# Optimization experiments

Measured on AMD Instinct MI355X. Metric: run time of the kernel, lower is better.

The kernel has to match this reference:

```python
import jax, jax.numpy as jnp
import numpy as np

B, L, D, NHEADS, P = 64, 256, 768, 8, 3
VOCAB, DEP, NLAYERS = 30522, 45, 2
LAM = 0.5


def _forward(src_mask, aspect_mask, lex, attention_mask,
             tok_emb, seg_emb, pool_w, pool_b, ln_a, ln_b,
             dep_emb, fc1_w, fc1_b, fc2_w, fc2_b,
             aq_w, aq_b, ak_w, ak_b, lq_w, lq_b, lk_w, lk_b, root_w,
             gcn_w, gcn_b, fc3_w, fc3_b, cls_w, cls_b, vlin_w,
             text_bert_indices, bert_segments_ids, ori_tag, head):
    b, l = text_bert_indices.shape
    d = tok_emb.shape[1]
    dk = d // NHEADS
    NEG = jnp.float32(-1e30)
    # stand-in BERT encoder: token + segment embeddings, tanh pooler on [CLS]
    seq = tok_emb[text_bert_indices] + seg_emb[bert_segments_ids]
    pooled = jnp.tanh(seq[:, 0] @ pool_w + pool_b)
    # torch LayerNorm variant: unbiased std (ddof=1)
    mean = seq.mean(-1, keepdims=True)
    std = jnp.std(seq, axis=-1, keepdims=True, ddof=1)
    gcn_in = ln_a * (seq - mean) / (std + 1e-6) + ln_b
    # in-place fmask[:,0]=1 mutates src_mask storage in torch -> effective mask
    sm = src_mask.at[:, 0].set(1.0)
    # dependency-tag score -> per-token softmax -> scatter into [L,L] adjacency
    dep_h = jax.nn.relu(dep_emb[ori_tag] @ fc1_w + fc1_b)
    dep_s = (dep_h @ fc2_w + fc2_b)[..., 0]                      # [B,L]
    dep_feat = jax.nn.softmax(dep_s * sm + (1.0 - sm) * NEG, axis=1)
    to_idx = jnp.arange(1, l)
    fro = head[:, :l - 1]                                        # [B,L-1]
    b_idx = jnp.arange(b)[:, None]
    vals = dep_feat[:, :l - 1]
    dep_adj = jnp.ones((b, l, l), jnp.float32)
    dep_adj = dep_adj.at[b_idx, fro, to_idx[None, :]].set(vals)
    dep_adj = dep_adj.at[b_idx, to_idx[None, :], fro].set(vals)
    # multi-head attention-as-adjacency (returns softmax weights only)
    q = (gcn_in @ aq_w + aq_b).reshape(b, l, NHEADS, dk).transpose(0, 2, 1, 3)
    k = (gcn_in @ ak_w + ak_b).reshape(b, l, NHEADS, dk).transpose(0, 2, 1, 3)
    scores = jnp.einsum('bhqd,bhkd->bhqk', q, k) / (jnp.sqrt(jnp.float32(dk)) + 1e-9)
    scores = jnp.where(sm[:, None, None, :] == 0, jnp.float32(-1e9), scores)
    adj_ag = jax.nn.softmax(scores, axis=-1).mean(axis=1)        # [B,L,L]
    eye = jnp.eye(l, dtype=jnp.float32)
    adj_ag = (adj_ag * (1.0 - eye) + eye) * sm[:, :, None]
    # structured latent attention (stand-in for missing StructuredAtt):
    # masked bilinear attention biased by dep_adj + root attention loss
    q2 = gcn_in @ lq_w + lq_b
    k2 = gcn_in @ lk_w + lk_b
    lat = jnp.einsum('bqd,bkd->bqk', q2, k2) / jnp.sqrt(jnp.float32(d))
    lat = lat + dep_adj + (1.0 - sm)[:, None, :] * (-10000.0)
    adj_latent = jax.nn.softmax(lat, axis=-1)
    root_p = jax.nn.softmax((gcn_in @ root_w)[..., 0] * sm + (1.0 - sm) * NEG, axis=1)
    loss_root = -jnp.mean(jnp.log(jnp.sum(root_p * aspect_mask, axis=1) + 1e-9))
    adj_latent = (adj_latent * (1.0 - eye) + eye) * sm[:, :, None]
    # gated dual-adjacency GCN layers
    H_l = gcn_in
    I_sem = gcn_in
    for layer in range(gcn_w.shape[0]):
        g_l = jax.nn.sigmoid(H_l)
        I_sem = (adj_ag @ H_l) @ gcn_w[layer] + gcn_b[layer]
        I_lat = (adj_latent @ H_l) @ gcn_w[layer] + gcn_b[layer]
        g = jax.nn.sigmoid(I_lat)
        lam_g = LAM * g
        I_com = (1.0 - lam_g) * I_sem + lam_g * I_lat
        H_out = jax.nn.relu(I_com @ fc3_w + fc3_b)
        H_l = g_l * H_out + (1.0 - g_l) * H_l
    # readout
    asp_wn = aspect_mask.sum(axis=1, keepdims=True)              # [B,1]
    m3 = sm[:, :, None]
    h_l = H_l * m3
    h_sem = I_sem * m3
    beta = jnp.einsum('bqd,bkd->bqk', h_l, h_sem) / 1000.0
    attn_o = jax.nn.softmax(beta.sum(axis=1, keepdims=True), axis=2)  # [B,1,L]
    outputs = (attn_o @ I_sem)[:, 0]                             # [B,D]
    sem_pool = (I_sem * aspect_mask[:, :, None]).sum(axis=1) / (asp_wn + 1e-9)
    final = jnp.concatenate([outputs, sem_pool, pooled], axis=-1)  # [B,3D]
    logits = final @ cls_w + cls_b
    e = (H_l @ vlin_w)[..., 0]
    lw = jax.nn.softmax(e, axis=1) * 50.0
    lw = lw * sm.at[:, 0].set(0.0)
    lexicon_loss = jnp.mean((lw - lex) ** 2)
    return logits, loss_root, lexicon_loss


def setup_inputs() -> dict:
    key = jax.random.key(0)
    ks = jax.random.split(key, 24)
    s = 0.02
    n = lambda i, shape: jax.random.normal(ks[i], shape, dtype=jnp.float32) * s
    inp = {}
    inp['text_bert_indices'] = jax.random.randint(ks[0], (B, L), 0, VOCAB, dtype=jnp.int32)
    inp['bert_segments_ids'] = jnp.zeros((B, L), jnp.int32)
    inp['attention_mask'] = jnp.ones((B, L), jnp.float32)
    inp['src_mask'] = jnp.ones((B, L), jnp.float32)
    inp['aspect_mask'] = jax.random.randint(ks[1], (B, L), 0, 2).astype(jnp.float32)
    inp['lex'] = jax.random.uniform(ks[2], (B, L), dtype=jnp.float32)
    inp['ori_tag'] = jax.random.randint(ks[3], (B, L), 0, DEP, dtype=jnp.int32)
    inp['head'] = jax.random.randint(ks[4], (B, L), 0, L, dtype=jnp.int32)
    inp['tok_emb'] = n(5, (VOCAB, D)); inp['seg_emb'] = n(6, (2, D))
    inp['pool_w'] = n(7, (D, D)); inp['pool_b'] = jnp.zeros((D,), jnp.float32)
    inp['ln_a'] = jnp.ones((D,), jnp.float32); inp['ln_b'] = jnp.zeros((D,), jnp.float32)
    inp['dep_emb'] = n(8, (DEP, 300))
    inp['fc1_w'] = n(9, (300, 256)); inp['fc1_b'] = jnp.zeros((256,), jnp.float32)
    inp['fc2_w'] = n(10, (256, 1)); inp['fc2_b'] = jnp.zeros((1,), jnp.float32)
    inp['aq_w'] = n(11, (D, D)); inp['aq_b'] = jnp.zeros((D,), jnp.float32)
    inp['ak_w'] = n(12, (D, D)); inp['ak_b'] = jnp.zeros((D,), jnp.float32)
    inp['lq_w'] = n(13, (D, D)); inp['lq_b'] = jnp.zeros((D,), jnp.float32)
    inp['lk_w'] = n(14, (D, D)); inp['lk_b'] = jnp.zeros((D,), jnp.float32)
    inp['root_w'] = n(15, (D, 1))
    inp['gcn_w'] = n(16, (NLAYERS, D, D)); inp['gcn_b'] = jnp.zeros((NLAYERS, D), jnp.float32)
    inp['fc3_w'] = n(17, (D, D)); inp['fc3_b'] = jnp.zeros((D,), jnp.float32)
    inp['cls_w'] = n(18, (3 * D, P)); inp['cls_b'] = jnp.zeros((P,), jnp.float32)
    inp['vlin_w'] = n(19, (D, 1))
    return inp


def reference(text_bert_indices, bert_segments_ids, attention_mask, src_mask, aspect_mask, lex,
              ori_tag, head, tok_emb, seg_emb, pool_w, pool_b, ln_a, ln_b, dep_emb,
              fc1_w, fc1_b, fc2_w, fc2_b, aq_w, aq_b, ak_w, ak_b, lq_w, lq_b, lk_w, lk_b,
              root_w, gcn_w, gcn_b, fc3_w, fc3_b, cls_w, cls_b, vlin_w):
    return _forward(src_mask, aspect_mask, lex, attention_mask,
                    tok_emb, seg_emb, pool_w, pool_b, ln_a, ln_b,
                    dep_emb, fc1_w, fc1_b, fc2_w, fc2_b,
                    aq_w, aq_b, ak_w, ak_b, lq_w, lq_b, lk_w, lk_b, root_w,
                    gcn_w, gcn_b, fc3_w, fc3_b, cls_w, cls_b, vlin_w,
                    text_bert_indices, bert_segments_ids, ori_tag, head)
```

## Files before the change

kernel.cpp:

```cpp
#include <hip/hip_runtime.h>
#include <hip/hip_bf16.h>
#include <math.h>

#define DI __device__ __forceinline__

constexpr int cB = 64, cL = 256, cD = 768;
constexpr long BLD = (long)cB * cL * cD;
constexpr long BLL = (long)cB * cL * cL;
constexpr long cLL = (long)cL * cL;
constexpr long cLD = (long)cL * cD;

typedef __attribute__((ext_vector_type(8))) short b8;
typedef __attribute__((ext_vector_type(4))) float f4;

#define GLDS(g, l)                                                    \
  __builtin_amdgcn_global_load_lds(                                   \
      (const __attribute__((address_space(1))) void*)(g),             \
      (__attribute__((address_space(3))) void*)(l), 16, 0, 0)

DI float wsum(float v) {
#pragma unroll
  for (int o = 32; o > 0; o >>= 1) v += __shfl_down(v, o, 64);
  return v;
}
DI float wsum_all(float v) {
#pragma unroll
  for (int m = 32; m > 0; m >>= 1) v += __shfl_xor(v, m, 64);
  return v;
}
DI float wmax_all(float v) {
#pragma unroll
  for (int m = 32; m > 0; m >>= 1) v = fmaxf(v, __shfl_xor(v, m, 64));
  return v;
}
DI float wmaxr(float v) {
#pragma unroll
  for (int o = 32; o > 0; o >>= 1) v = fmaxf(v, __shfl_down(v, o, 64));
  return v;
}
DI float blockSum(float v) {
  __shared__ float sh[4];
  v = wsum(v);
  __syncthreads();
  if ((threadIdx.x & 63) == 0) sh[threadIdx.x >> 6] = v;
  __syncthreads();
  return sh[0] + sh[1] + sh[2] + sh[3];
}
DI float blockMax(float v) {
  __shared__ float sh[4];
  v = wmaxr(v);
  __syncthreads();
  if ((threadIdx.x & 63) == 0) sh[threadIdx.x >> 6] = v;
  __syncthreads();
  return fmaxf(fmaxf(sh[0], sh[1]), fmaxf(sh[2], sh[3]));
}
DI float sigf(float x) { return 1.f / (1.f + expf(-x)); }

template <int OBF, int RELU, int BIAS, int EPI>
__global__ __launch_bounds__(256, 2) void bgemm(
    const __hip_bfloat16* __restrict__ A, const __hip_bfloat16* __restrict__ BT,
    void* __restrict__ Cv, const float* __restrict__ bias,
    float* __restrict__ auxf, __hip_bfloat16* __restrict__ auxb,
    int K, int lda, int ldb, int ldc,
    int zshift, int zmask, long sA1, long sA2, long sB1, long sB2, long sC,
    int czdiv) {
  __shared__ __hip_bfloat16 Asp[128 * 32];
  __shared__ __hip_bfloat16 Bsp[128 * 32];
  int z = blockIdx.z;
  A += (long)(z >> zshift) * sA1 + (long)(z & zmask) * sA2;
  BT += (long)(z >> zshift) * sB1 + (long)(z & zmask) * sB2;
  int tid = threadIdx.x;
  int lane = tid & 63, w = tid >> 6;
  int wr = w >> 1, wc = w & 1;
  int l16 = lane & 15, q = lane >> 4;
  int m0 = blockIdx.y << 7, n0 = blockIdx.x << 7;

  int fm = tid >> 2, fq = tid & 3;
  const __hip_bfloat16* Ap0 = A + (long)(m0 + fm) * lda + fq * 8;
  const __hip_bfloat16* Ap1 = A + (long)(m0 + fm + 64) * lda + fq * 8;
  const __hip_bfloat16* Bp0 = BT + (long)(n0 + fm) * ldb + fq * 8;
  const __hip_bfloat16* Bp1 = BT + (long)(n0 + fm + 64) * ldb + fq * 8;
  char* Aw0 = (char*)Asp + (w << 10);
  char* Aw1 = (char*)Asp + 4096 + (w << 10);
  char* Bw0 = (char*)Bsp + (w << 10);
  char* Bw1 = (char*)Bsp + 4096 + (w << 10);

  f4 acc[4][4];
#pragma unroll
  for (int i = 0; i < 4; i++)
#pragma unroll
    for (int j = 0; j < 4; j++) acc[i][j] = (f4){0.f, 0.f, 0.f, 0.f};

  for (int k0 = 0; k0 < K; k0 += 32) {
    GLDS(Ap0 + k0, Aw0);
    GLDS(Ap1 + k0, Aw1);
    GLDS(Bp0 + k0, Bw0);
    GLDS(Bp1 + k0, Bw1);
    __syncthreads();
    b8 af[4], bf[4];
#pragma unroll
    for (int i = 0; i < 4; i++)
      af[i] = *(const b8*)&Asp[(wr * 64 + i * 16 + l16) * 32 + q * 8];
#pragma unroll
    for (int j = 0; j < 4; j++)
      bf[j] = *(const b8*)&Bsp[(wc * 64 + j * 16 + l16) * 32 + q * 8];
#pragma unroll
    for (int i = 0; i < 4; i++)
#pragma unroll
      for (int j = 0; j < 4; j++)
        acc[i][j] = __builtin_amdgcn_mfma_f32_16x16x32_bf16(af[i], bf[j], acc[i][j], 0, 0, 0);
    __syncthreads();
  }
  if (EPI == 4) {
#pragma unroll
    for (int j = 0; j < 4; j++) {
      int n = n0 + wc * 64 + j * 16 + l16;
#pragma unroll
      for (int i = 0; i < 4; i++) {
        int m = m0 + wr * 64 + i * 16 + (q << 2);
        __hip_bfloat16 t4[4];
#pragma unroll
        for (int r = 0; r < 4; r++) t4[r] = __float2bfloat16(acc[i][j][r]);
        long bidx = (long)(m >> 8) * sC + (long)n * cL + (m & 255);
        *(uint2*)&((__hip_bfloat16*)Cv)[bidx] = *(uint2*)t4;
      }
    }
    return;
  }
  long cz = (long)(z >> czdiv) * sC;
#pragma unroll
  for (int j = 0; j < 4; j++) {
    int n = n0 + wc * 64 + j * 16 + l16;
    float bv = BIAS ? bias[n] : 0.f;
#pragma unroll
    for (int i = 0; i < 4; i++) {
#pragma unroll
      for (int r = 0; r < 4; r++) {
        int m = m0 + wr * 64 + i * 16 + q * 4 + r;
        long idx = cz + (long)m * ldc + n;
        float v = acc[i][j][r] + bv;
        if (EPI == 0) {
          if (RELU) v = fmaxf(v, 0.f);
          if (OBF)
            ((__hip_bfloat16*)Cv)[idx] = __float2bfloat16(v);
          else
            ((float*)Cv)[idx] = v;
        } else {
          v = fmaxf(v, 0.f);
          float h = __bfloat162float(auxb[idx]);
          float g = sigf(h);
          float o = h + g * (v - h);
          auxb[idx] = __float2bfloat16(o);
          if (auxf) auxf[idx] = o;
        }
      }
    }
  }
}

__global__ __launch_bounds__(256, 2) void bgemm_dual(
    const __hip_bfloat16* __restrict__ A1g, const __hip_bfloat16* __restrict__ A2g,
    const __hip_bfloat16* __restrict__ BTg, float* __restrict__ IsemF,
    __hip_bfloat16* __restrict__ Icb, const float* __restrict__ bias,
    int write_isem) {
  __shared__ __hip_bfloat16 A1sp[128 * 32];
  __shared__ __hip_bfloat16 A2sp[128 * 32];
  __shared__ __hip_bfloat16 Bsp[128 * 32];
  int z = blockIdx.z;
  const __hip_bfloat16* A1 = A1g + (long)z * cLL;
  const __hip_bfloat16* A2 = A2g + (long)z * cLL;
  const __hip_bfloat16* BT = BTg + (long)z * cLD;
  int tid = threadIdx.x;
  int lane = tid & 63, w = tid >> 6;
  int wr = w >> 1, wc = w & 1;
  int l16 = lane & 15, q = lane >> 4;
  int m0 = blockIdx.y << 7, n0 = blockIdx.x << 7;

  int fm = tid >> 2, fq = tid & 3;
  const __hip_bfloat16* A1p0 = A1 + (long)(m0 + fm) * cL + fq * 8;
  const __hip_bfloat16* A1p1 = A1p0 + 64L * cL;
  const __hip_bfloat16* A2p0 = A2 + (long)(m0 + fm) * cL + fq * 8;
  const __hip_bfloat16* A2p1 = A2p0 + 64L * cL;
  const __hip_bfloat16* Bp0 = BT + (long)(n0 + fm) * cL + fq * 8;
  const __hip_bfloat16* Bp1 = Bp0 + 64L * cL;
  char* w10 = (char*)A1sp + (w << 10);
  char* w11 = (char*)A1sp + 4096 + (w << 10);
  char* w20 = (char*)A2sp + (w << 10);
  char* w21 = (char*)A2sp + 4096 + (w << 10);
  char* wb0 = (char*)Bsp + (w << 10);
  char* wb1 = (char*)Bsp + 4096 + (w << 10);

  f4 ac1[4][4], ac2[4][4];
#pragma unroll
  for (int i = 0; i < 4; i++)
#pragma unroll
    for (int j = 0; j < 4; j++) {
      ac1[i][j] = (f4){0.f, 0.f, 0.f, 0.f};
      ac2[i][j] = (f4){0.f, 0.f, 0.f, 0.f};
    }

  for (int k0 = 0; k0 < cL; k0 += 32) {
    GLDS(A1p0 + k0, w10);
    GLDS(A1p1 + k0, w11);
    GLDS(A2p0 + k0, w20);
    GLDS(A2p1 + k0, w21);
    GLDS(Bp0 + k0, wb0);
    GLDS(Bp1 + k0, wb1);
    __syncthreads();
    b8 a1f[4], a2f[4], bf[4];
#pragma unroll
    for (int i = 0; i < 4; i++) {
      a1f[i] = *(const b8*)&A1sp[(wr * 64 + i * 16 + l16) * 32 + q * 8];
      a2f[i] = *(const b8*)&A2sp[(wr * 64 + i * 16 + l16) * 32 + q * 8];
    }
#pragma unroll
    for (int j = 0; j < 4; j++)
      bf[j] = *(const b8*)&Bsp[(wc * 64 + j * 16 + l16) * 32 + q * 8];
#pragma unroll
    for (int i = 0; i < 4; i++)
#pragma unroll
      for (int j = 0; j < 4; j++) {
        ac1[i][j] = __builtin_amdgcn_mfma_f32_16x16x32_bf16(a1f[i], bf[j], ac1[i][j], 0, 0, 0);
        ac2[i][j] = __builtin_amdgcn_mfma_f32_16x16x32_bf16(a2f[i], bf[j], ac2[i][j], 0, 0, 0);
      }
    __syncthreads();
  }
  long cz = (long)z * cLD;
#pragma unroll
  for (int j = 0; j < 4; j++) {
    int n = n0 + wc * 64 + j * 16 + l16;
    float bv = bias[n];
#pragma unroll
    for (int i = 0; i < 4; i++) {
#pragma unroll
      for (int r = 0; r < 4; r++) {
        int m = m0 + wr * 64 + i * 16 + q * 4 + r;
        long idx = cz + (long)m * cD + n;
        float is = ac1[i][j][r] + bv;
        float il = ac2[i][j][r] + bv;
        float g = 0.5f * sigf(il);
        Icb[idx] = __float2bfloat16(is + g * (il - is));
        if (write_isem) IsemF[idx] = is;
      }
    }
  }
}

template <int NH>
__global__ __launch_bounds__(256, 2) void k_qkadj(
    const __hip_bfloat16* __restrict__ qkb, const float* __restrict__ src_mask,
    const int* __restrict__ headv, const float* __restrict__ df,
    __hip_bfloat16* __restrict__ outA) {
  constexpr int KH = (NH == 8) ? 96 : 768;
  constexpr int QOFF = (NH == 8) ? 0 : 1536;
  constexpr int KOFF = (NH == 8) ? 768 : 2304;
  const float scale = (NH == 8) ? (1.f / (sqrtf(96.f) + 1e-9f)) : (1.f / sqrtf(768.f));
  __shared__ __hip_bfloat16 Qs[64 * 32];
  __shared__ __hip_bfloat16 Ks[256 * 32];
  __shared__ float red[4][64];
  const int b = blockIdx.y, m0 = blockIdx.x << 6;
  const int tid = threadIdx.x, lane = tid & 63, w = tid >> 6;
  const int l16 = lane & 15, q = lane >> 4;
  const long rowbase = (long)b * cL;
  const __hip_bfloat16* Qg = qkb + (rowbase + m0 + (tid >> 2)) * 3072 + (tid & 3) * 8 + QOFF;
  const __hip_bfloat16* Kg = qkb + (rowbase + (tid >> 2)) * 3072 + (tid & 3) * 8 + KOFF;
  char* qdst = (char*)Qs + (w << 10);

  float smj[4];
  int hcol[4];
  float dfc[4];
#pragma unroll
  for (int j = 0; j < 4; j++) {
    int col = w * 64 + j * 16 + l16;
    smj[j] = (col == 0) ? 1.f : src_mask[b * cL + col];
    if (NH == 1) {
      hcol[j] = (col >= 1) ? headv[b * cL + col - 1] : -1;
      dfc[j] = (col >= 1) ? df[b * cL + col - 1] : 0.f;
    }
  }
  float smi_[4][4];
  int hrow_[4][4];
  float dfr_[4][4];
#pragma unroll
  for (int i = 0; i < 4; i++)
#pragma unroll
    for (int r = 0; r < 4; r++) {
      int grow = m0 + i * 16 + q * 4 + r;
      smi_[i][r] = (grow == 0) ? 1.f : src_mask[b * cL + grow];
      if (NH == 1) {
        hrow_[i][r] = (grow >= 1) ? headv[b * cL + grow - 1] : -1;
        dfr_[i][r] = (grow >= 1) ? df[b * cL + grow - 1] : 0.f;
      }
    }

  f4 aag[4][4];
#pragma unroll
  for (int i = 0; i < 4; i++)
#pragma unroll
    for (int j = 0; j < 4; j++) aag[i][j] = (f4){0.f, 0.f, 0.f, 0.f};

  f4 sa[4][4];
  float inv_[4][4];
  for (int h = 0; h < NH; h++) {
    const int hk = h * 96;
#pragma unroll
    for (int i = 0; i < 4; i++)
#pragma unroll
      for (int j = 0; j < 4; j++) sa[i][j] = (f4){0.f, 0.f, 0.f, 0.f};
    for (int k0 = 0; k0 < KH; k0 += 32) {
      __syncthreads();
      GLDS(Qg + hk + k0, qdst);
#pragma unroll
      for (int u = 0; u < 4; u++)
        GLDS(Kg + (long)u * 196608 + hk + k0, (char*)Ks + u * 4096 + (w << 10));
      __syncthreads();
      b8 af[4], bf[4];
#pragma unroll
      for (int i = 0; i < 4; i++)
        af[i] = *(const b8*)&Qs[(i * 16 + l16) * 32 + q * 8];
#pragma unroll
      for (int j = 0; j < 4; j++)
        bf[j] = *(const b8*)&Ks[(w * 64 + j * 16 + l16) * 32 + q * 8];
#pragma unroll
      for (int i = 0; i < 4; i++)
#pragma unroll
        for (int j = 0; j < 4; j++)
          sa[i][j] = __builtin_amdgcn_mfma_f32_16x16x32_bf16(af[i], bf[j], sa[i][j], 0, 0, 0);
    }
#pragma unroll
    for (int i = 0; i < 4; i++)
#pragma unroll
      for (int j = 0; j < 4; j++)
#pragma unroll
        for (int r = 0; r < 4; r++) {
          float raw = sa[i][j][r];
          float v;
          if (NH == 1) {
            int grow = m0 + i * 16 + q * 4 + r;
            int col = w * 64 + j * 16 + l16;
            float dep = 1.f;
            if (hcol[j] == grow) dep = dfc[j];
            if (col == hrow_[i][r]) dep = dfr_[i][r];
            v = raw * scale + dep + (1.f - smj[j]) * -10000.f;
          } else {
            v = (smj[j] == 0.f) ? -1e9f : raw * scale;
          }
          sa[i][j][r] = v;
        }
    float rm_[4][4];
#pragma unroll
    for (int i = 0; i < 4; i++)
#pragma unroll
      for (int r = 0; r < 4; r++) {
        float m = fmaxf(fmaxf(sa[i][0][r], sa[i][1][r]), fmaxf(sa[i][2][r], sa[i][3][r]));
#pragma unroll
        for (int o = 1; o < 16; o <<= 1) m = fmaxf(m, __shfl_xor(m, o, 64));
        if (l16 == 0) red[w][i * 16 + q * 4 + r] = m;
        rm_[i][r] = m;
      }
    __syncthreads();
#pragma unroll
    for (int i = 0; i < 4; i++)
#pragma unroll
      for (int r = 0; r < 4; r++) {
        int lr = i * 16 + q * 4 + r;
        rm_[i][r] = fmaxf(fmaxf(red[0][lr], red[1][lr]), fmaxf(red[2][lr], red[3][lr]));
      }
    __syncthreads();
#pragma unroll
    for (int i = 0; i < 4; i++)
#pragma unroll
      for (int r = 0; r < 4; r++) {
        float s0 = 0.f;
#pragma unroll
        for (int j = 0; j < 4; j++) {
          float e = expf(sa[i][j][r] - rm_[i][r]);
          sa[i][j][r] = e;
          s0 += e;
        }
#pragma unroll
        for (int o = 1; o < 16; o <<= 1) s0 += __shfl_xor(s0, o, 64);
        if (l16 == 0) red[w][i * 16 + q * 4 + r] = s0;
      }
    __syncthreads();
#pragma unroll
    for (int i = 0; i < 4; i++)
#pragma unroll
      for (int r = 0; r < 4; r++) {
        int lr = i * 16 + q * 4 + r;
        inv_[i][r] = 1.f / (red[0][lr] + red[1][lr] + red[2][lr] + red[3][lr]);
      }
    if (NH == 8) {
#pragma unroll
      for (int i = 0; i < 4; i++)
#pragma unroll
        for (int j = 0; j < 4; j++)
#pragma unroll
          for (int r = 0; r < 4; r++) aag[i][j][r] += sa[i][j][r] * inv_[i][r];
    }
  }
#pragma unroll
  for (int j = 0; j < 4; j++) {
    int col = w * 64 + j * 16 + l16;
#pragma unroll
    for (int i = 0; i < 4; i++)
#pragma unroll
      for (int r = 0; r < 4; r++) {
        int grow = m0 + i * 16 + q * 4 + r;
        float p = (NH == 8) ? aag[i][j][r] * 0.125f : sa[i][j][r] * inv_[i][r];
        float v = (col == grow) ? 1.f : p;
        outA[((long)b * cL + grow) * cL + col] = __float2bfloat16(v * smi_[i][r]);
      }
  }
}

__global__ void k_wconv7(const float* __restrict__ s0, const float* __restrict__ s1,
                         const float* __restrict__ s2, const float* __restrict__ s3,
                         const float* __restrict__ s4, const float* __restrict__ s5,
                         const float* __restrict__ s6, __hip_bfloat16* __restrict__ dst) {
  const float* srcs[7] = {s0, s1, s2, s3, s4, s5, s6};
  const float* src = srcs[blockIdx.z];
  __hip_bfloat16* d = dst + (long)blockIdx.z * cD * cD;
  __shared__ float t[32][33];
  int k0 = blockIdx.x * 32, n0 = blockIdx.y * 32;
  int tx = threadIdx.x, ty = threadIdx.y;
#pragma unroll
  for (int i = 0; i < 32; i += 8) t[ty + i][tx] = src[(long)(k0 + ty + i) * cD + n0 + tx];
  __syncthreads();
#pragma unroll
  for (int i = 0; i < 32; i += 8)
    d[(long)(n0 + ty + i) * cD + k0 + tx] = __float2bfloat16(t[tx][ty + i]);
}

__global__ __launch_bounds__(256) void k_gcnin(
    const int* __restrict__ tbi, const int* __restrict__ bsi,
    const float* __restrict__ tok, const float* __restrict__ seg,
    const float* __restrict__ ln_a, const float* __restrict__ ln_b,
    const float* __restrict__ root_w, __hip_bfloat16* __restrict__ gib,
    float* __restrict__ x64, float* __restrict__ e1) {
  int wave = threadIdx.x >> 6, lane = threadIdx.x & 63;
  long bl = (long)blockIdx.x * 4 + wave;
  int t = tbi[bl], s = bsi[bl];
  const float* tr = tok + (long)t * cD;
  const float* sr = seg + (long)s * cD;
  float x[12];
  float ls = 0.f;
#pragma unroll
  for (int c = 0; c < 12; c++) {
    int d = lane + (c << 6);
    x[c] = tr[d] + sr[d];
    ls += x[c];
  }
  if ((bl & 255) == 0) {
#pragma unroll
    for (int c = 0; c < 12; c++) x64[(bl >> 8) * cD + lane + (c << 6)] = x[c];
  }
  float mean = wsum_all(ls) * (1.f / 768.f);
  float lv = 0.f;
#pragma unroll
  for (int c = 0; c < 12; c++) { float d2 = x[c] - mean; lv += d2 * d2; }
  float var = wsum_all(lv) * (1.f / 767.f);
  float inv = 1.f / (sqrtf(var) + 1e-6f);
  float rdot = 0.f;
#pragma unroll
  for (int c = 0; c < 12; c++) {
    int d = lane + (c << 6);
    float v = ln_a[d] * (x[c] - mean) * inv + ln_b[d];
    gib[bl * cD + d] = __float2bfloat16(v);
    rdot += v * root_w[d];
  }
  float tot = wsum_all(rdot);
  if (lane == 0) e1[bl] = tot;
}

__global__ __launch_bounds__(256) void k_pool1(
    const float* __restrict__ x64, const float* __restrict__ pw,
    float* __restrict__ pacc) {
  __shared__ float pws[48][256];
  __shared__ float xs[16][48];
  int i0 = blockIdx.x * 48, j0 = blockIdx.y * 256, b0 = blockIdx.z * 16;
  for (int r = 0; r < 48; r++) pws[r][threadIdx.x] = pw[(long)(i0 + r) * cD + j0 + threadIdx.x];
  for (int idx = threadIdx.x; idx < 16 * 48; idx += 256)
    xs[idx / 48][idx % 48] = x64[(long)(b0 + idx / 48) * cD + i0 + idx % 48];
  __syncthreads();
  int j = threadIdx.x;
  for (int b = 0; b < 16; b++) {
    float acc = 0.f;
#pragma unroll 8
    for (int i = 0; i < 48; i++) acc += xs[b][i] * pws[i][j];
    atomicAdd(&pacc[(long)(b0 + b) * cD + j0 + j], acc);
  }
}
__global__ __launch_bounds__(256) void k_pool2(
    const float* __restrict__ pacc, const float* __restrict__ pb,
    float* __restrict__ pooled) {
  int b = blockIdx.x;
#pragma unroll
  for (int c = 0; c < 3; c++) {
    int j = (c << 8) + threadIdx.x;
    pooled[(long)b * cD + j] = tanhf(pacc[(long)b * cD + j] + pb[j]);
  }
}

__global__ __launch_bounds__(256) void k_s45(
    const float* __restrict__ dep_emb, const float* __restrict__ fc1w,
    const float* __restrict__ fc1b, const float* __restrict__ fc2w,
    const float* __restrict__ fc2b, float* __restrict__ s45) {
  int t = blockIdx.x;
  __shared__ float e[300];
  for (int i = threadIdx.x; i < 300; i += 256) e[i] = dep_emb[t * 300 + i];
  __syncthreads();
  int j = threadIdx.x;
  float h = fc1b[j];
  for (int i = 0; i < 300; i++) h += e[i] * fc1w[i * 256 + j];
  h = fmaxf(h, 0.f);
  float tot = blockSum(h * fc2w[j]);
  if (threadIdx.x == 0) s45[t] = tot + fc2b[0];
}

__global__ __launch_bounds__(256) void k_depfeat(
    const int* __restrict__ ori, const float* __restrict__ src_mask,
    const float* __restrict__ s45, float* __restrict__ dep_feat) {
  int b = blockIdx.x, l = threadIdx.x;
  float smv = (l == 0) ? 1.f : src_mask[b * cL + l];
  float sc = s45[ori[b * cL + l]] * smv + (1.f - smv) * (-1e30f);
  float mx = blockMax(sc);
  float ex = expf(sc - mx);
  float sum = blockSum(ex);
  dep_feat[b * cL + l] = ex / sum;
}

__global__ void k_bcat(const float* __restrict__ a, const float* __restrict__ b,
                       const float* __restrict__ c, const float* __restrict__ d,
                       float* __restrict__ o) {
  int i = blockIdx.x * 256 + threadIdx.x;
  float v = (i < 768) ? a[i] : (i < 1536) ? b[i - 768] : (i < 2304) ? c[i - 1536] : d[i - 2304];
  o[i] = v;
}

__global__ __launch_bounds__(256) void k_rowdot(
    const float* __restrict__ X, const float* __restrict__ w, long wstride,
    float* __restrict__ e) {
  int r = blockIdx.x * 4 + (threadIdx.x >> 6);
  int lane = threadIdx.x & 63;
  const float4* row = (const float4*)(X + (long)r * cD);
  const float4* wp = (const float4*)(w + (long)(r >> 8) * wstride);
  float s = 0.f;
#pragma unroll
  for (int c = 0; c < 3; c++) {
    int idx = c * 64 + lane;
    float4 a = row[idx], b = wp[idx];
    s += a.x * b.x + a.y * b.y + a.z * b.z + a.w * b.w;
  }
  s = wsum(s);
  if (lane == 0) e[r] = s;
}

__global__ __launch_bounds__(256) void k_root2(
    const float* __restrict__ e1, const float* __restrict__ src_mask,
    const float* __restrict__ aspect_mask, float* __restrict__ out_loss) {
  int b = blockIdx.x, l = threadIdx.x;
  float r = e1[b * cL + l];
  float smv = (l == 0) ? 1.f : src_mask[b * cL + l];
  float sc = r * smv + (1.f - smv) * (-1e30f);
  float mx = blockMax(sc);
  float ex = expf(sc - mx);
  float sum = blockSum(ex);
  float p = ex / sum;
  float tot = blockSum(p * aspect_mask[b * cL + l]);
  if (l == 0) atomicAdd(out_loss, -logf(tot + 1e-9f) * (1.f / 64.f));
}

__global__ __launch_bounds__(256) void k_lex2(
    const float* __restrict__ e2, const float* __restrict__ src_mask,
    const float* __restrict__ lex, float* __restrict__ out_loss) {
  int b = blockIdx.x, l = threadIdx.x;
  float e = e2[b * cL + l];
  float mx = blockMax(e);
  float ex = expf(e - mx);
  float sum = blockSum(ex);
  float mult = (l == 0) ? 0.f : src_mask[b * cL + l];
  float lw = ex / sum * 50.f * mult;
  float d2 = lw - lex[b * cL + l];
  float tot = blockSum(d2 * d2);
  if (l == 0) atomicAdd(out_loss, tot * (1.f / (64.f * 256.f)));
}

__global__ __launch_bounds__(256) void k_hl(
    const float* __restrict__ H, const float* __restrict__ src_mask,
    float* __restrict__ hlsum) {
  int b = blockIdx.z, d = (blockIdx.y << 8) + threadIdx.x, l0 = blockIdx.x * 32;
  float acc = 0.f;
  for (int l = l0; l < l0 + 32; l++) {
    float smv = (l == 0) ? 1.f : src_mask[b * cL + l];
    acc += H[((long)b * cL + l) * cD + d] * smv;
  }
  atomicAdd(&hlsum[(long)b * cD + d], acc);
}

__global__ __launch_bounds__(256) void k_attnw(
    const float* __restrict__ sraw, const float* __restrict__ src_mask,
    const float* __restrict__ am, float* __restrict__ wgt, float* __restrict__ asum) {
  int b = blockIdx.x, k = threadIdx.x;
  float smk = (k == 0) ? 1.f : src_mask[b * cL + k];
  float s = sraw[b * cL + k] * smk * 0.001f;
  float mx = blockMax(s);
  float ex = expf(s - mx);
  float sum = blockSum(ex);
  wgt[b * cL + k] = ex / sum;
  float a = blockSum(am[b * cL + k]);
  if (k == 0) asum[b] = a;
}

__global__ __launch_bounds__(256) void k_wsum(
    const float* __restrict__ Isem, const float* __restrict__ wgt,
    const float* __restrict__ am, float* __restrict__ outputs,
    float* __restrict__ sempool) {
  int b = blockIdx.z, d = (blockIdx.y << 8) + threadIdx.x, l0 = blockIdx.x * 32;
  float accO = 0.f, accS = 0.f;
  for (int l = l0; l < l0 + 32; l++) {
    float v = Isem[((long)b * cL + l) * cD + d];
    accO += wgt[b * cL + l] * v;
    accS += am[b * cL + l] * v;
  }
  atomicAdd(&outputs[(long)b * cD + d], accO);
  atomicAdd(&sempool[(long)b * cD + d], accS);
}

__global__ __launch_bounds__(256) void k_logits(
    const float* __restrict__ outputs, const float* __restrict__ sempool,
    const float* __restrict__ pooled, const float* __restrict__ asum,
    const float* __restrict__ cw, const float* __restrict__ cb,
    float* __restrict__ out) {
  int b = blockIdx.x;
  float inv = 1.f / (asum[b] + 1e-9f);
  float a0 = 0.f, a1 = 0.f, a2 = 0.f;
  for (int i = threadIdx.x; i < 3 * cD; i += 256) {
    float f = (i < cD) ? outputs[(long)b * cD + i]
              : (i < 2 * cD) ? sempool[(long)b * cD + i - cD] * inv
                             : pooled[(long)b * cD + i - 2 * cD];
    a0 += f * cw[i * 3 + 0];
    a1 += f * cw[i * 3 + 1];
    a2 += f * cw[i * 3 + 2];
  }
  a0 = blockSum(a0);
  a1 = blockSum(a1);
  a2 = blockSum(a2);
  if (threadIdx.x == 0) {
    out[b * 3 + 0] = a0 + cb[0];
    out[b * 3 + 1] = a1 + cb[1];
    out[b * 3 + 2] = a2 + cb[2];
  }
}

extern "C" void kernel_launch(void* const* d_in, const int* in_sizes, int n_in,
                              void* d_out, int out_size, void* d_ws, size_t ws_size,
                              hipStream_t stream) {
  const int* tbi = (const int*)d_in[0];
  const int* bsi = (const int*)d_in[1];
  const float* src_mask = (const float*)d_in[3];
  const float* aspect_mask = (const float*)d_in[4];
  const float* lex = (const float*)d_in[5];
  const int* ori = (const int*)d_in[6];
  const int* head = (const int*)d_in[7];
  const float* tok_emb = (const float*)d_in[8];
  const float* seg_emb = (const float*)d_in[9];
  const float* pool_w = (const float*)d_in[10];
  const float* pool_b = (const float*)d_in[11];
  const float* ln_a = (const float*)d_in[12];
  const float* ln_b = (const float*)d_in[13];
  const float* dep_emb = (const float*)d_in[14];
  const float* fc1_w = (const float*)d_in[15];
  const float* fc1_b = (const float*)d_in[16];
  const float* fc2_w = (const float*)d_in[17];
  const float* fc2_b = (const float*)d_in[18];
  const float* aq_w = (const float*)d_in[19];
  const float* aq_b = (const float*)d_in[20];
  const float* ak_w = (const float*)d_in[21];
  const float* ak_b = (const float*)d_in[22];
  const float* lq_w = (const float*)d_in[23];
  const float* lq_b = (const float*)d_in[24];
  const float* lk_w = (const float*)d_in[25];
  const float* lk_b = (const float*)d_in[26];
  const float* root_w = (const float*)d_in[27];
  const float* gcn_w = (const float*)d_in[28];
  const float* gcn_b = (const float*)d_in[29];
  const float* fc3_w = (const float*)d_in[30];
  const float* fc3_b = (const float*)d_in[31];
  const float* cls_w = (const float*)d_in[32];
  const float* cls_b = (const float*)d_in[33];
  const float* vlin_w = (const float*)d_in[34];

  float* out = (float*)d_out;
  float* ws = (float*)d_ws;
  float* gcnH = ws;
  float* Isem = gcnH + BLD;
  float* depfeat = Isem + BLD;
  float* s45 = depfeat + cB * cL;
  float* pooled = s45 + 64;
  float* x64 = pooled + cB * cD;
  float* hlsum = x64 + cB * cD;
  float* outputs = hlsum + cB * cD;
  float* sempool = outputs + cB * cD;
  float* pacc = sempool + cB * cD;
  float* e1 = pacc + cB * cD;
  float* e2 = e1 + cB * cL;
  float* sraw = e2 + cB * cL;
  float* wgt = sraw + cB * cL;
  float* asum = wgt + cB * cL;
  float* catb = asum + 64;
  __hip_bfloat16* gib = (__hip_bfloat16*)(catb + 3072);
  __hip_bfloat16* qkb = gib + BLD;
  __hip_bfloat16* scores = qkb + 4 * BLD;
  __hip_bfloat16* adjag_b = scores + 8 * BLL;
  __hip_bfloat16* adjlat_b = adjag_b + BLL;
  __hip_bfloat16* wbt = adjlat_b + BLL;
  __hip_bfloat16* HWbT = qkb + BLD;
  __hip_bfloat16* Icb = qkb + 2 * BLD;

  hipMemsetAsync((char*)d_out + 192 * sizeof(float), 0, 2 * sizeof(float), stream);
  hipMemsetAsync(hlsum, 0, 4 * cB * cD * sizeof(float), stream);

  k_gcnin<<<cB * cL / 4, 256, 0, stream>>>(tbi, bsi, tok_emb, seg_emb, ln_a, ln_b,
                                           root_w, gib, x64, e1);
  k_s45<<<45, 256, 0, stream>>>(dep_emb, fc1_w, fc1_b, fc2_w, fc2_b, s45);
  k_depfeat<<<cB, 256, 0, stream>>>(ori, src_mask, s45, depfeat);
  k_pool1<<<dim3(16, 3, 4), 256, 0, stream>>>(x64, pool_w, pacc);
  k_pool2<<<cB, 256, 0, stream>>>(pacc, pool_b, pooled);
  k_bcat<<<12, 256, 0, stream>>>(aq_b, ak_b, lq_b, lk_b, catb);
  k_wconv7<<<dim3(24, 24, 7), dim3(32, 8), 0, stream>>>(
      aq_w, ak_w, lq_w, lk_w, gcn_w, gcn_w + (long)cD * cD, fc3_w, wbt);

  const long DD = (long)cD * cD;
  const long LD = cLD;

  bgemm<1, 0, 1, 0><<<dim3(24, 128, 1), 256, 0, stream>>>(
      gib, wbt, qkb, catb, nullptr, nullptr, cD, cD, cD, 3072,
      0, 0, 0, 0, 0, 0, 0, 0);

  k_qkadj<8><<<dim3(4, cB), 256, 0, stream>>>(qkb, src_mask, nullptr, nullptr, adjag_b);
  k_qkadj<1><<<dim3(4, cB), 256, 0, stream>>>(qkb, src_mask, head, depfeat, adjlat_b);

  k_root2<<<cB, 256, 0, stream>>>(e1, src_mask, aspect_mask, out + 192);

  for (int layer = 0; layer < 2; layer++) {
    const float* bb = gcn_b + (long)layer * cD;
    bgemm<1, 0, 0, 4><<<dim3(6, 128, 1), 256, 0, stream>>>(
        gib, wbt + (4 + layer) * DD, HWbT, nullptr, nullptr, nullptr,
        cD, cD, cD, cD, 0, 0, 0, 0, 0, 0, LD, 0);
    bgemm_dual<<<dim3(6, 2, cB), 256, 0, stream>>>(
        adjag_b, adjlat_b, HWbT, Isem, Icb, bb, layer == 1 ? 1 : 0);
    bgemm<0, 1, 1, 2><<<dim3(6, 128, 1), 256, 0, stream>>>(
        Icb, wbt + 6 * DD, nullptr, fc3_b, layer == 1 ? gcnH : nullptr, gib,
        cD, cD, cD, cD, 0, 0, 0, 0, 0, 0, 0, 0);
  }

  k_hl<<<dim3(8, 3, cB), 256, 0, stream>>>(gcnH, src_mask, hlsum);
  k_rowdot<<<cB * cL / 4, 256, 0, stream>>>(Isem, hlsum, cD, sraw);
  k_attnw<<<cB, 256, 0, stream>>>(sraw, src_mask, aspect_mask, wgt, asum);
  k_wsum<<<dim3(8, 3, cB), 256, 0, stream>>>(Isem, wgt, aspect_mask, outputs, sempool);
  k_logits<<<cB, 256, 0, stream>>>(outputs, sempool, pooled, asum, cls_w, cls_b, out);
  k_rowdot<<<cB * cL / 4, 256, 0, stream>>>(gcnH, vlin_w, 0, e2);
  k_lex2<<<cB, 256, 0, stream>>>(e2, src_mask, lex, out + 193);
}
```

Baseline: 807.0 us.

## Fuse small tail kernels, merge qkadj launches, and swizzle GEMM block order

Several small launches are folded together. k_pool2 moves into k_logits, k_bcat into k_wconv7, and the two k_qkadj template launches become one grid split on z. The two rowdot launches share one kernel, and root, attention-weight and lex reductions run in one tail kernel. The GEMM kernels also get a block-index swizzle that interleaves tiles in groups of 8, meant to improve cache locality across the GPU's chiplets. The main goal is fewer launches and better L2 reuse, at the cost of runtime branching in the merged qkadj kernel, which may raise register pressure.

```diff
diff --git a/kernel.cpp b/kernel.cpp
--- a/kernel.cpp
+++ b/kernel.cpp
@@ -26,11 +26,6 @@
 DI float wsum_all(float v) {
 #pragma unroll
   for (int m = 32; m > 0; m >>= 1) v += __shfl_xor(v, m, 64);
-  return v;
-}
-DI float wmax_all(float v) {
-#pragma unroll
-  for (int m = 32; m > 0; m >>= 1) v = fmaxf(v, __shfl_xor(v, m, 64));
   return v;
 }
 DI float wmaxr(float v) {
@@ -56,7 +51,7 @@
 }
 DI float sigf(float x) { return 1.f / (1.f + expf(-x)); }
 
-template <int OBF, int RELU, int BIAS, int EPI>
+template <int OBF, int RELU, int BIAS, int EPI, int SWZ>
 __global__ __launch_bounds__(256, 2) void bgemm(
     const __hip_bfloat16* __restrict__ A, const __hip_bfloat16* __restrict__ BT,
     void* __restrict__ Cv, const float* __restrict__ bias,
@@ -66,6 +61,16 @@
     int czdiv) {
   __shared__ __hip_bfloat16 Asp[128 * 32];
   __shared__ __hip_bfloat16 Bsp[128 * 32];
+  int bx = blockIdx.x, by = blockIdx.y;
+  if (SWZ) {
+    int gx = gridDim.x;
+    int nb = gx * gridDim.y;
+    int id = by * gx + bx;
+    int cpx = nb >> 3;
+    id = (id & 7) * cpx + (id >> 3);
+    bx = id % gx;
+    by = id / gx;
+  }
   int z = blockIdx.z;
   A += (long)(z >> zshift) * sA1 + (long)(z & zmask) * sA2;
   BT += (long)(z >> zshift) * sB1 + (long)(z & zmask) * sB2;
@@ -73,7 +78,7 @@
   int lane = tid & 63, w = tid >> 6;
   int wr = w >> 1, wc = w & 1;
   int l16 = lane & 15, q = lane >> 4;
-  int m0 = blockIdx.y << 7, n0 = blockIdx.x << 7;
+  int m0 = by << 7, n0 = bx << 7;
 
   int fm = tid >> 2, fq = tid & 3;
   const __hip_bfloat16* Ap0 = A + (long)(m0 + fm) * lda + fq * 8;
@@ -166,7 +171,10 @@
   __shared__ __hip_bfloat16 A1sp[128 * 32];
   __shared__ __hip_bfloat16 A2sp[128 * 32];
   __shared__ __hip_bfloat16 Bsp[128 * 32];
-  int z = blockIdx.z;
+  int id = (blockIdx.z * 2 + blockIdx.y) * 6 + blockIdx.x;
+  id = (id & 7) * 96 + (id >> 3);
+  int bx = id % 6, t = id / 6;
+  int by = t & 1, z = t >> 1;
   const __hip_bfloat16* A1 = A1g + (long)z * cLL;
   const __hip_bfloat16* A2 = A2g + (long)z * cLL;
   const __hip_bfloat16* BT = BTg + (long)z * cLD;
@@ -174,7 +182,7 @@
   int lane = tid & 63, w = tid >> 6;
   int wr = w >> 1, wc = w & 1;
   int l16 = lane & 15, q = lane >> 4;
-  int m0 = blockIdx.y << 7, n0 = blockIdx.x << 7;
+  int m0 = by << 7, n0 = bx << 7;
 
   int fm = tid >> 2, fq = tid & 3;
   const __hip_bfloat16* A1p0 = A1 + (long)(m0 + fm) * cL + fq * 8;
@@ -246,15 +254,16 @@
   }
 }
 
-template <int NH>
-__global__ __launch_bounds__(256, 2) void k_qkadj(
+__global__ __launch_bounds__(256, 2) void k_qkadj2(
     const __hip_bfloat16* __restrict__ qkb, const float* __restrict__ src_mask,
     const int* __restrict__ headv, const float* __restrict__ df,
-    __hip_bfloat16* __restrict__ outA) {
-  constexpr int KH = (NH == 8) ? 96 : 768;
-  constexpr int QOFF = (NH == 8) ? 0 : 1536;
-  constexpr int KOFF = (NH == 8) ? 768 : 2304;
-  const float scale = (NH == 8) ? (1.f / (sqrtf(96.f) + 1e-9f)) : (1.f / sqrtf(768.f));
+    __hip_bfloat16* __restrict__ outAag, __hip_bfloat16* __restrict__ outAlat) {
+  const bool lat = blockIdx.z != 0;
+  const int NH = lat ? 1 : 8;
+  const int KH = lat ? 768 : 96;
+  const int QOFF = lat ? 1536 : 0;
+  const int KOFF = lat ? 2304 : 768;
+  const float scale = lat ? (1.f / sqrtf(768.f)) : (1.f / (sqrtf(96.f) + 1e-9f));
   __shared__ __hip_bfloat16 Qs[64 * 32];
   __shared__ __hip_bfloat16 Ks[256 * 32];
   __shared__ float red[4][64];
@@ -273,7 +282,7 @@
   for (int j = 0; j < 4; j++) {
     int col = w * 64 + j * 16 + l16;
     smj[j] = (col == 0) ? 1.f : src_mask[b * cL + col];
-    if (NH == 1) {
+    if (lat) {
       hcol[j] = (col >= 1) ? headv[b * cL + col - 1] : -1;
       dfc[j] = (col >= 1) ? df[b * cL + col - 1] : 0.f;
     }
@@ -287,7 +296,7 @@
     for (int r = 0; r < 4; r++) {
       int grow = m0 + i * 16 + q * 4 + r;
       smi_[i][r] = (grow == 0) ? 1.f : src_mask[b * cL + grow];
-      if (NH == 1) {
+      if (lat) {
         hrow_[i][r] = (grow >= 1) ? headv[b * cL + grow - 1] : -1;
         dfr_[i][r] = (grow >= 1) ? df[b * cL + grow - 1] : 0.f;
       }
@@ -335,7 +344,7 @@
         for (int r = 0; r < 4; r++) {
           float raw = sa[i][j][r];
           float v;
-          if (NH == 1) {
+          if (lat) {
             int grow = m0 + i * 16 + q * 4 + r;
             int col = w * 64 + j * 16 + l16;
             float dep = 1.f;
@@ -390,7 +399,7 @@
         int lr = i * 16 + q * 4 + r;
         inv_[i][r] = 1.f / (red[0][lr] + red[1][lr] + red[2][lr] + red[3][lr]);
       }
-    if (NH == 8) {
+    if (!lat) {
 #pragma unroll
       for (int i = 0; i < 4; i++)
 #pragma unroll
@@ -399,6 +408,7 @@
           for (int r = 0; r < 4; r++) aag[i][j][r] += sa[i][j][r] * inv_[i][r];
     }
   }
+  __hip_bfloat16* outA = lat ? outAlat : outAag;
 #pragma unroll
   for (int j = 0; j < 4; j++) {
     int col = w * 64 + j * 16 + l16;
@@ -407,7 +417,7 @@
 #pragma unroll
       for (int r = 0; r < 4; r++) {
         int grow = m0 + i * 16 + q * 4 + r;
-        float p = (NH == 8) ? aag[i][j][r] * 0.125f : sa[i][j][r] * inv_[i][r];
+        float p = lat ? sa[i][j][r] * inv_[i][r] : aag[i][j][r] * 0.125f;
         float v = (col == grow) ? 1.f : p;
         outA[((long)b * cL + grow) * cL + col] = __float2bfloat16(v * smi_[i][r]);
       }
@@ -417,7 +427,19 @@
 __global__ void k_wconv7(const float* __restrict__ s0, const float* __restrict__ s1,
                          const float* __restrict__ s2, const float* __restrict__ s3,
                          const float* __restrict__ s4, const float* __restrict__ s5,
-                         const float* __restrict__ s6, __hip_bfloat16* __restrict__ dst) {
+                         const float* __restrict__ s6, __hip_bfloat16* __restrict__ dst,
+                         const float* __restrict__ ba, const float* __restrict__ bb,
+                         const float* __restrict__ bc, const float* __restrict__ bd,
+                         float* __restrict__ catb) {
+  if (blockIdx.z == 7) {
+    if (blockIdx.y != 0 || blockIdx.x >= 12) return;
+    int tid = threadIdx.y * 32 + threadIdx.x;
+    int i = blockIdx.x * 256 + tid;
+    float v = (i < 768) ? ba[i] : (i < 1536) ? bb[i - 768]
+              : (i < 2304) ? bc[i - 1536] : bd[i - 2304];
+    catb[i] = v;
+    return;
+  }
   const float* srcs[7] = {s0, s1, s2, s3, s4, s5, s6};
   const float* src = srcs[blockIdx.z];
   __hip_bfloat16* d = dst + (long)blockIdx.z * cD * cD;
@@ -491,16 +513,6 @@
     atomicAdd(&pacc[(long)(b0 + b) * cD + j0 + j], acc);
   }
 }
-__global__ __launch_bounds__(256) void k_pool2(
-    const float* __restrict__ pacc, const float* __restrict__ pb,
-    float* __restrict__ pooled) {
-  int b = blockIdx.x;
-#pragma unroll
-  for (int c = 0; c < 3; c++) {
-    int j = (c << 8) + threadIdx.x;
-    pooled[(long)b * cD + j] = tanhf(pacc[(long)b * cD + j] + pb[j]);
-  }
-}
 
 __global__ __launch_bounds__(256) void k_s45(
     const float* __restrict__ dep_emb, const float* __restrict__ fc1w,
@@ -530,21 +542,16 @@
   dep_feat[b * cL + l] = ex / sum;
 }
 
-__global__ void k_bcat(const float* __restrict__ a, const float* __restrict__ b,
-                       const float* __restrict__ c, const float* __restrict__ d,
-                       float* __restrict__ o) {
-  int i = blockIdx.x * 256 + threadIdx.x;
-  float v = (i < 768) ? a[i] : (i < 1536) ? b[i - 768] : (i < 2304) ? c[i - 1536] : d[i - 2304];
-  o[i] = v;
-}
-
-__global__ __launch_bounds__(256) void k_rowdot(
-    const float* __restrict__ X, const float* __restrict__ w, long wstride,
-    float* __restrict__ e) {
+__global__ __launch_bounds__(256) void k_rowdot2(
+    const float* __restrict__ Isem, const float* __restrict__ hlsum,
+    const float* __restrict__ gcnH, const float* __restrict__ vlin,
+    float* __restrict__ sraw, float* __restrict__ e2) {
   int r = blockIdx.x * 4 + (threadIdx.x >> 6);
   int lane = threadIdx.x & 63;
-  const float4* row = (const float4*)(X + (long)r * cD);
-  const float4* wp = (const float4*)(w + (long)(r >> 8) * wstride);
+  bool z = blockIdx.y != 0;
+  const float4* row = (const float4*)((z ? gcnH : Isem) + (long)r * cD);
+  const float4* wp = z ? (const float4*)vlin
+                       : (const float4*)(hlsum + (long)(r >> 8) * cD);
   float s = 0.f;
 #pragma unroll
   for (int c = 0; c < 3; c++) {
@@ -553,37 +560,40 @@
     s += a.x * b.x + a.y * b.y + a.z * b.z + a.w * b.w;
   }
   s = wsum(s);
-  if (lane == 0) e[r] = s;
-}
-
-__global__ __launch_bounds__(256) void k_root2(
-    const float* __restrict__ e1, const float* __restrict__ src_mask,
-    const float* __restrict__ aspect_mask, float* __restrict__ out_loss) {
+  if (lane == 0) (z ? e2 : sraw)[r] = s;
+}
+
+__global__ __launch_bounds__(256) void k_tailred(
+    const float* __restrict__ sraw, const float* __restrict__ e1,
+    const float* __restrict__ e2, const float* __restrict__ src_mask,
+    const float* __restrict__ aspect_mask, const float* __restrict__ lex,
+    float* __restrict__ wgt, float* __restrict__ asum,
+    float* __restrict__ out_root, float* __restrict__ out_lex) {
   int b = blockIdx.x, l = threadIdx.x;
-  float r = e1[b * cL + l];
   float smv = (l == 0) ? 1.f : src_mask[b * cL + l];
-  float sc = r * smv + (1.f - smv) * (-1e30f);
-  float mx = blockMax(sc);
-  float ex = expf(sc - mx);
+  float am = aspect_mask[b * cL + l];
+  float s = sraw[b * cL + l] * smv * 0.001f;
+  float mx = blockMax(s);
+  float ex = expf(s - mx);
   float sum = blockSum(ex);
-  float p = ex / sum;
-  float tot = blockSum(p * aspect_mask[b * cL + l]);
-  if (l == 0) atomicAdd(out_loss, -logf(tot + 1e-9f) * (1.f / 64.f));
-}
-
-__global__ __launch_bounds__(256) void k_lex2(
-    const float* __restrict__ e2, const float* __restrict__ src_mask,
-    const float* __restrict__ lex, float* __restrict__ out_loss) {
-  int b = blockIdx.x, l = threadIdx.x;
+  wgt[b * cL + l] = ex / sum;
+  float a = blockSum(am);
+  if (l == 0) asum[b] = a;
+  float sc = e1[b * cL + l] * smv + (1.f - smv) * (-1e30f);
+  float mx2 = blockMax(sc);
+  float ex2 = expf(sc - mx2);
+  float sum2 = blockSum(ex2);
+  float tot = blockSum((ex2 / sum2) * am);
+  if (l == 0) atomicAdd(out_root, -logf(tot + 1e-9f) * (1.f / 64.f));
   float e = e2[b * cL + l];
-  float mx = blockMax(e);
-  float ex = expf(e - mx);
-  float sum = blockSum(ex);
+  float mx3 = blockMax(e);
+  float ex3 = expf(e - mx3);
+  float sum3 = blockSum(ex3);
   float mult = (l == 0) ? 0.f : src_mask[b * cL + l];
-  float lw = ex / sum * 50.f * mult;
+  float lw = ex3 / sum3 * 50.f * mult;
   float d2 = lw - lex[b * cL + l];
-  float tot = blockSum(d2 * d2);
-  if (l == 0) atomicAdd(out_loss, tot * (1.f / (64.f * 256.f)));
+  float t3 = blockSum(d2 * d2);
+  if (l == 0) atomicAdd(out_lex, t3 * (1.f / (64.f * 256.f)));
 }
 
 __global__ __launch_bounds__(256) void k_hl(
@@ -596,20 +606,6 @@
     acc += H[((long)b * cL + l) * cD + d] * smv;
   }
   atomicAdd(&hlsum[(long)b * cD + d], acc);
-}
-
-__global__ __launch_bounds__(256) void k_attnw(
-    const float* __restrict__ sraw, const float* __restrict__ src_mask,
-    const float* __restrict__ am, float* __restrict__ wgt, float* __restrict__ asum) {
-  int b = blockIdx.x, k = threadIdx.x;
-  float smk = (k == 0) ? 1.f : src_mask[b * cL + k];
-  float s = sraw[b * cL + k] * smk * 0.001f;
-  float mx = blockMax(s);
-  float ex = expf(s - mx);
-  float sum = blockSum(ex);
-  wgt[b * cL + k] = ex / sum;
-  float a = blockSum(am[b * cL + k]);
-  if (k == 0) asum[b] = a;
 }
 
 __global__ __launch_bounds__(256) void k_wsum(
@@ -629,16 +625,20 @@
 
 __global__ __launch_bounds__(256) void k_logits(
     const float* __restrict__ outputs, const float* __restrict__ sempool,
-    const float* __restrict__ pooled, const float* __restrict__ asum,
-    const float* __restrict__ cw, const float* __restrict__ cb,
-    float* __restrict__ out) {
+    const float* __restrict__ pacc, const float* __restrict__ pb,
+    const float* __restrict__ asum, const float* __restrict__ cw,
+    const float* __restrict__ cb, float* __restrict__ out) {
   int b = blockIdx.x;
   float inv = 1.f / (asum[b] + 1e-9f);
   float a0 = 0.f, a1 = 0.f, a2 = 0.f;
   for (int i = threadIdx.x; i < 3 * cD; i += 256) {
-    float f = (i < cD) ? outputs[(long)b * cD + i]
-              : (i < 2 * cD) ? sempool[(long)b * cD + i - cD] * inv
-                             : pooled[(long)b * cD + i - 2 * cD];
+    float f;
+    if (i < cD)
+      f = outputs[(long)b * cD + i];
+    else if (i < 2 * cD)
+      f = sempool[(long)b * cD + i - cD] * inv;
+    else
+      f = tanhf(pacc[(long)b * cD + i - 2 * cD] + pb[i - 2 * cD]);
     a0 += f * cw[i * 3 + 0];
     a1 += f * cw[i * 3 + 1];
     a2 += f * cw[i * 3 + 2];
@@ -726,40 +726,38 @@
   k_s45<<<45, 256, 0, stream>>>(dep_emb, fc1_w, fc1_b, fc2_w, fc2_b, s45);
   k_depfeat<<<cB, 256, 0, stream>>>(ori, src_mask, s45, depfeat);
   k_pool1<<<dim3(16, 3, 4), 256, 0, stream>>>(x64, pool_w, pacc);
-  k_pool2<<<cB, 256, 0, stream>>>(pacc, pool_b, pooled);
-  k_bcat<<<12, 256, 0, stream>>>(aq_b, ak_b, lq_b, lk_b, catb);
-  k_wconv7<<<dim3(24, 24, 7), dim3(32, 8), 0, stream>>>(
-      aq_w, ak_w, lq_w, lk_w, gcn_w, gcn_w + (long)cD * cD, fc3_w, wbt);
+  k_wconv7<<<dim3(24, 24, 8), dim3(32, 8), 0, stream>>>(
+      aq_w, ak_w, lq_w, lk_w, gcn_w, gcn_w + (long)cD * cD, fc3_w, wbt,
+      aq_b, ak_b, lq_b, lk_b, catb);
 
   const long DD = (long)cD * cD;
   const long LD = cLD;
 
-  bgemm<1, 0, 1, 0><<<dim3(24, 128, 1), 256, 0, stream>>>(
+  bgemm<1, 0, 1, 0, 1><<<dim3(24, 128, 1), 256, 0, stream>>>(
       gib, wbt, qkb, catb, nullptr, nullptr, cD, cD, cD, 3072,
       0, 0, 0, 0, 0, 0, 0, 0);
 
-  k_qkadj<8><<<dim3(4, cB), 256, 0, stream>>>(qkb, src_mask, nullptr, nullptr, adjag_b);
-  k_qkadj<1><<<dim3(4, cB), 256, 0, stream>>>(qkb, src_mask, head, depfeat, adjlat_b);
-
-  k_root2<<<cB, 256, 0, stream>>>(e1, src_mask, aspect_mask, out + 192);
+  k_qkadj2<<<dim3(4, cB, 2), 256, 0, stream>>>(qkb, src_mask, head, depfeat,
+                                               adjag_b, adjlat_b);
 
   for (int layer = 0; layer < 2; layer++) {
     const float* bb = gcn_b + (long)layer * cD;
-    bgemm<1, 0, 0, 4><<<dim3(6, 128, 1), 256, 0, stream>>>(
+    bgemm<1, 0, 0, 4, 1><<<dim3(6, 128, 1), 256, 0, stream>>>(
         gib, wbt + (4 + layer) * DD, HWbT, nullptr, nullptr, nullptr,
         cD, cD, cD, cD, 0, 0, 0, 0, 0, 0, LD, 0);
     bgemm_dual<<<dim3(6, 2, cB), 256, 0, stream>>>(
         adjag_b, adjlat_b, HWbT, Isem, Icb, bb, layer == 1 ? 1 : 0);
-    bgemm<0, 1, 1, 2><<<dim3(6, 128, 1), 256, 0, stream>>>(
+    bgemm<0, 1, 1, 2, 1><<<dim3(6, 128, 1), 256, 0, stream>>>(
         Icb, wbt + 6 * DD, nullptr, fc3_b, layer == 1 ? gcnH : nullptr, gib,
         cD, cD, cD, cD, 0, 0, 0, 0, 0, 0, 0, 0);
   }
 
   k_hl<<<dim3(8, 3, cB), 256, 0, stream>>>(gcnH, src_mask, hlsum);
-  k_rowdot<<<cB * cL / 4, 256, 0, stream>>>(Isem, hlsum, cD, sraw);
-  k_attnw<<<cB, 256, 0, stream>>>(sraw, src_mask, aspect_mask, wgt, asum);
+  k_rowdot2<<<dim3(cB * cL / 4, 2), 256, 0, stream>>>(Isem, hlsum, gcnH, vlin_w,
+                                                      sraw, e2);
+  k_tailred<<<cB, 256, 0, stream>>>(sraw, e1, e2, src_mask, aspect_mask, lex,
+                                    wgt, asum, out + 192, out + 193);
   k_wsum<<<dim3(8, 3, cB), 256, 0, stream>>>(Isem, wgt, aspect_mask, outputs, sempool);
-  k_logits<<<cB, 256, 0, stream>>>(outputs, sempool, pooled, asum, cls_w, cls_b, out);
-  k_rowdot<<<cB * cL / 4, 256, 0, stream>>>(gcnH, vlin_w, 0, e2);
-  k_lex2<<<cB, 256, 0, stream>>>(e2, src_mask, lex, out + 193);
-}
+  k_logits<<<cB, 256, 0, stream>>>(outputs, sempool, pacc, pool_b, asum,
+                                   cls_w, cls_b, out);
+}
```

New measurement: 802.3 us. About the same (-0.6%).
